# Optimization experiments

Measured on AMD Instinct MI355X. Metric: run time of the kernel, lower is better.

The kernel has to match this reference:

```python
import jax, jax.numpy as jnp
import numpy as np

ALPHA = 0.1   # leaky integration rate
NOISE = 0.02  # noise std
B, T, I, H, O = 64, 512, 128, 1024, 64


def setup_inputs() -> dict:
    key = jax.random.key(0)
    k1, k2, k3, k4, k5 = jax.random.split(key, 5)
    x = jax.random.normal(k1, (B, T, I), dtype=jnp.float32)
    wi = jax.random.normal(k2, (I, H), dtype=jnp.float32) / np.sqrt(I).astype(np.float32)
    wrec = jax.random.normal(k3, (H, H), dtype=jnp.float32) / np.sqrt(H).astype(np.float32)
    wo = jax.random.normal(k4, (H, O), dtype=jnp.float32) / np.sqrt(H).astype(np.float32)
    noise = jax.random.normal(k5, (B, T, H), dtype=jnp.float32)  # pre-sampled standard normal
    return {"x": x, "noise": noise, "wi": wi, "wrec": wrec, "wo": wo}


def reference(x, noise, wi, wrec, wo):
    # x: [B,T,I], noise: [B,T,H]; leaky tanh RNN scanned over time.
    batch = x.shape[0]
    h0 = jnp.zeros((batch, wrec.shape[0]), dtype=x.dtype)
    xs = jnp.swapaxes(x, 0, 1)       # [T,B,I]
    ns = jnpp if False else jnp.swapaxes(noise, 0, 1)  # [T,B,H]

    def step(h, inp):
        xt, nt = inp
        h = (1.0 - ALPHA) * h + ALPHA * (xt @ wi + jnp.tanh(h) @ wrec + nt * NOISE)
        return h, jnp.tanh(h) @ wo   # per-step output [B,O]

    _, outs = jax.lax.scan(step, h0, (xs, ns))  # outs: [T,B,O]
    return jnp.swapaxes(outs, 0, 1)  # [B,T,O]
```

## Files before the change

### kernel.cpp

```cpp
#include <hip/hip_runtime.h>
#include <hip/hip_bf16.h>


#define T_ 512
#define I_ 128
#define H_ 1024
#define O_ 64
#define GRPS 4
#define BG 16
#define WPG 32
#define NWG 128
#define POLL_CAP (1<<17)

#define GBUF_BYTES (GRPS*2*BG*H_*2)
#define STEPFLAG_OFF GBUF_BYTES
#define WS_NEED (GBUF_BYTES + 1024)

#define WREC_HI_E 0
#define WREC_LO_E 32768
#define WI_HI_E   65536
#define WI_LO_E   69632
#define WO_HI_E   73728
#define WO_LO_E   75776
#define RED_B     155648
#define REDO_B    161792
#define LDS_BYTES 162176

typedef __bf16 bf16x8 __attribute__((ext_vector_type(8)));
typedef float f32x4 __attribute__((ext_vector_type(4)));
typedef unsigned u32x4 __attribute__((ext_vector_type(4)));
typedef unsigned short u16;

__device__ __forceinline__ float fast_tanh(float v){
  float cx = fminf(fmaxf(v, -14.f), 14.f);
  float e = __builtin_amdgcn_exp2f(cx * 2.8853900817779268f);
  return 1.f - 2.f * __builtin_amdgcn_rcpf(e + 1.f);
}

__device__ __forceinline__ void flag_issue(unsigned& v, const u16* p){
  asm volatile("global_load_ushort %0, %1, off sc0 sc1" : "=v"(v) : "v"(p));
}
__device__ __forceinline__ unsigned sflag_load(const u16* p){
  unsigned v;
  asm volatile("global_load_ushort %0, %1, off sc0 sc1\n\ts_waitcnt vmcnt(0)"
               : "=v"(v) : "v"(p) : "memory");
  return v;
}
__device__ __forceinline__ void sflag_store(u16* p, unsigned v){
  asm volatile("global_store_short %0, %1, off sc0 sc1" :: "v"(p), "v"(v) : "memory");
}
__device__ __forceinline__ void g_load_frag(u32x4& d, const u16* p){
  asm volatile("global_load_dwordx4 %0, %1, off sc0 sc1" : "=v"(d) : "v"(p));
}
__device__ __forceinline__ void g_store_u16(u16* p, unsigned v){
  asm volatile("global_store_short %0, %1, off sc0 sc1" :: "v"(p), "v"(v) : "memory");
}
__device__ __forceinline__ void g_store_f32(float* p, float v){
  asm volatile("global_store_dword %0, %1, off" :: "v"(p), "v"(v) : "memory");
}
__device__ __forceinline__ void gl_f32x4(f32x4& d, const float* p){
  asm volatile("global_load_dwordx4 %0, %1, off" : "=v"(d) : "v"(p));
}
__device__ __forceinline__ void gl_f32(float& d, const float* p){
  asm volatile("global_load_dword %0, %1, off" : "=v"(d) : "v"(p));
}
__device__ __forceinline__ void barrier_lds(){
  asm volatile("s_waitcnt lgkmcnt(0)\n\ts_barrier" ::: "memory");
}

__device__ void load_slice(const float* __restrict__ Wg, int ld, int c0, int K,
                           __bf16* hi, __bf16* lo){
  for (int idx = threadIdx.x; idx < K*32; idx += 256){
    int k = idx >> 5, c = idx & 31;
    float v = Wg[(size_t)k*ld + c0 + c];
    __bf16 h = (__bf16)v;
    __bf16 l = (__bf16)(v - (float)h);
    int kt = k >> 5, kin = k & 31, lg = kin >> 3, j = kin & 7;
    int off = (((kt*2 + (c>>4))*64 + (lg*16 + (c&15))) << 3) + j;
    hi[off] = h; lo[off] = l;
  }
}

#define MFMA __builtin_amdgcn_mfma_f32_16x16x32_bf16
#define BC(u) __builtin_bit_cast(bf16x8, u)

#define PACKX(v0, v1, xh, xl)                                      \
  { _Pragma("unroll")                                              \
    for (int jj = 0; jj < 4; ++jj){                                \
      float aa = (v0)[jj], bb = (v1)[jj];                          \
      __bf16 ah = (__bf16)aa, bh2 = (__bf16)bb;                    \
      (xh)[jj] = ah; (xh)[jj+4] = bh2;                             \
      (xl)[jj] = (__bf16)(aa - (float)ah);                         \
      (xl)[jj+4] = (__bf16)(bb - (float)bh2); } }

extern "C" __global__ __launch_bounds__(256, 1)
void rnn_kernel(const float* __restrict__ x, const float* __restrict__ noise,
                const float* __restrict__ wi, const float* __restrict__ wrec,
                const float* __restrict__ wo, float* __restrict__ out,
                u16* __restrict__ gbuf, u16* __restrict__ sflags)
{
  extern __shared__ char smem[];
  __bf16* B = (__bf16*)smem;
  float* REDN = (float*)(smem + RED_B);
  float* REDO = (float*)(smem + REDO_B);

  const int grp  = blockIdx.x >> 5;
  const int role = blockIdx.x & 31;
  const int c0 = role * 32;

  load_slice(wrec, H_, c0, H_, B + WREC_HI_E, B + WREC_LO_E);
  load_slice(wi,   H_, c0, I_, B + WI_HI_E,  B + WI_LO_E);
  for (int idx = threadIdx.x; idx < 2*H_; idx += 256){
    int col = idx >> 10, k = idx & (H_-1);
    float v = wo[(size_t)k*O_ + role*2 + col];
    __bf16 hh = (__bf16)v;
    B[WO_HI_E + col*H_ + k] = hh;
    B[WO_LO_E + col*H_ + k] = (__bf16)(v - (float)hh);
  }
  __syncthreads();

  const int lane = threadIdx.x & 63;
  const int w    = threadIdx.x >> 6;
  const int lhalf = lane >> 4;
  const int l15   = lane & 15;
  const int bf = lane * 8;
  const int wo_off = (l15 & 1)*1024 + lhalf*8;

  u16* gg = gbuf + grp * (2*BG*H_);
  u16* gf = sflags + grp * 64;
  const u16* pollp = gf + lane;
  const u16* abase = gg + (size_t)l15*H_ + w*256 + lhalf*8;

  const float* xrow  = x + (size_t)(grp*BG + l15)*T_*I_ + lhalf*8;
  const float* nrow0 = noise + (size_t)(grp*BG + lhalf*4)*T_*H_ + c0 + (w&1)*16 + l15;
  float* orow = out + (size_t)(grp*BG + lhalf*4)*T_*O_ + role*2 + (l15 & 1);

  f32x4 h0 = {0.f,0.f,0.f,0.f};
  f32x4 xA = {0.f,0.f,0.f,0.f}, xB = {0.f,0.f,0.f,0.f};
  u32x4 a[8];
  f32x4 xv[8];
  float nz[4] = {0.f,0.f,0.f,0.f};

  if (w < 2){
    gl_f32x4(xv[0], xrow);      gl_f32x4(xv[1], xrow+4);
    gl_f32x4(xv[2], xrow+32);   gl_f32x4(xv[3], xrow+36);
    gl_f32x4(xv[4], xrow+64);   gl_f32x4(xv[5], xrow+68);
    gl_f32x4(xv[6], xrow+96);   gl_f32x4(xv[7], xrow+100);
    asm volatile("s_waitcnt vmcnt(0)"
      : "+v"(xv[0]),"+v"(xv[1]),"+v"(xv[2]),"+v"(xv[3]),
        "+v"(xv[4]),"+v"(xv[5]),"+v"(xv[6]),"+v"(xv[7]));
    __builtin_amdgcn_sched_barrier(0);
    #pragma unroll
    for (int kt = 0; kt < 4; ++kt){
      bf16x8 xh, xl; PACKX(xv[kt*2], xv[kt*2+1], xh, xl);
      bf16x8 wih = *(const bf16x8*)(B + WI_HI_E + kt*1024 + w*512 + bf);
      bf16x8 wil = *(const bf16x8*)(B + WI_LO_E + kt*1024 + w*512 + bf);
      xA = MFMA(xh, wih, xA, 0,0,0);
      xB = MFMA(xl, wih, xB, 0,0,0);
      xA = MFMA(xh, wil, xA, 0,0,0);
    }
    const float* xp = xrow + I_;
    gl_f32x4(xv[0], xp);      gl_f32x4(xv[1], xp+4);
    gl_f32x4(xv[2], xp+32);   gl_f32x4(xv[3], xp+36);
    gl_f32x4(xv[4], xp+64);   gl_f32x4(xv[5], xp+68);
    gl_f32x4(xv[6], xp+96);   gl_f32x4(xv[7], xp+100);
    gl_f32(nz[0], nrow0);
    gl_f32(nz[1], nrow0 + (size_t)T_*H_);
    gl_f32(nz[2], nrow0 + (size_t)2*T_*H_);
    gl_f32(nz[3], nrow0 + (size_t)3*T_*H_);
  }
  #pragma unroll
  for (int kt = 0; kt < 8; ++kt) g_load_frag(a[kt], abase + kt*32);

  for (int i = 0; i < T_; ++i){
    f32x4 c0A={0.f,0.f,0.f,0.f}, c0B={0.f,0.f,0.f,0.f};
    f32x4 c1A={0.f,0.f,0.f,0.f}, c1B={0.f,0.f,0.f,0.f};
    f32x4 oA ={0.f,0.f,0.f,0.f}, oB ={0.f,0.f,0.f,0.f};
    if (w == 0){ c0A = xA; c0B = xB; }
    if (w == 1){ c1A = xA; c1B = xB; }
    const int kb = w*8;
#define CSTEP(KT, N)                                                          \
    { asm volatile("s_waitcnt vmcnt(" #N ")" : "+v"(a[KT]));                  \
      __builtin_amdgcn_sched_barrier(0);                                      \
      const int kg = kb + KT;                                                 \
      bf16x8 av = BC(a[KT]);                                                  \
      bf16x8 bh0 = *(const bf16x8*)(B + WREC_HI_E + kg*1024 + bf);            \
      bf16x8 bl0 = *(const bf16x8*)(B + WREC_LO_E + kg*1024 + bf);            \
      bf16x8 bh1 = *(const bf16x8*)(B + WREC_HI_E + kg*1024 + 512 + bf);      \
      bf16x8 bl1 = *(const bf16x8*)(B + WREC_LO_E + kg*1024 + 512 + bf);      \
      bf16x8 wh  = *(const bf16x8*)(B + WO_HI_E + wo_off + kg*32);            \
      bf16x8 wl  = *(const bf16x8*)(B + WO_LO_E + wo_off + kg*32);            \
      c0A = MFMA(av, bh0, c0A, 0,0,0);  c0B = MFMA(av, bl0, c0B, 0,0,0);      \
      c1A = MFMA(av, bh1, c1A, 0,0,0);  c1B = MFMA(av, bl1, c1B, 0,0,0);      \
      oA  = MFMA(av, wh,  oA,  0,0,0);  oB  = MFMA(av, wl,  oB,  0,0,0); }
    CSTEP(0,7) CSTEP(1,6) CSTEP(2,5) CSTEP(3,4)
    CSTEP(4,3) CSTEP(5,2) CSTEP(6,1) CSTEP(7,0)
#undef CSTEP
    f32x4 cn0 = c0A + c0B, cn1 = c1A + c1B, co = oA + oB;

    if (w == 0){ *(f32x4*)&REDN[((1*3+0)*64+lane)*4] = cn1;
                 if (l15 < 2) *(f32x4*)&REDO[(0*8 + lhalf*2 + l15)*4] = co; }
    if (w == 1){ *(f32x4*)&REDN[((0*3+0)*64+lane)*4] = cn0;
                 if (l15 < 2) *(f32x4*)&REDO[(1*8 + lhalf*2 + l15)*4] = co; }
    if (w == 2){ *(f32x4*)&REDN[((0*3+1)*64+lane)*4] = cn0;
                 *(f32x4*)&REDN[((1*3+1)*64+lane)*4] = cn1; }
    if (w == 3){ *(f32x4*)&REDN[((0*3+2)*64+lane)*4] = cn0;
                 *(f32x4*)&REDN[((1*3+2)*64+lane)*4] = cn1;
                 if (l15 < 2) *(f32x4*)&REDO[(2*8 + lhalf*2 + l15)*4] = co; }
    barrier_lds();

    if (w < 2){
      const int fb = w ? 3 : 0;
      f32x4 s = w ? cn1 : cn0;
      s += *(f32x4*)&REDN[((fb+0)*64+lane)*4];
      s += *(f32x4*)&REDN[((fb+1)*64+lane)*4];
      s += *(f32x4*)&REDN[((fb+2)*64+lane)*4];
      u16* gp = gg + (size_t)((i+1)&1)*(BG*H_);
      #pragma unroll
      for (int r = 0; r < 4; ++r){
        int row = lhalf*4 + r;
        float hv = 0.9f*h0[r] + 0.1f*s[r] + 0.002f*nz[r];
        h0[r] = hv;
        u16 gv = __builtin_bit_cast(u16, (__bf16)fast_tanh(hv));
        g_store_u16(gp + (size_t)row*H_ + c0 + w*16 + l15, (unsigned)gv);
      }
    } else if (w == 2 && i > 0 && l15 < 2){
      f32x4 s = co;
      s += *(f32x4*)&REDO[(0*8 + lhalf*2 + l15)*4];
      s += *(f32x4*)&REDO[(1*8 + lhalf*2 + l15)*4];
      s += *(f32x4*)&REDO[(2*8 + lhalf*2 + l15)*4];
      #pragma unroll
      for (int r = 0; r < 4; ++r)
        g_store_f32(orow + (size_t)r*T_*O_ + (size_t)(i-1)*O_, s[r]);
    }

    if (w < 2){
      asm volatile("s_waitcnt vmcnt(0)" ::: "memory");
      if (lane == 0) sflag_store(gf + role*2 + w, (unsigned)(i+1));
    }

    unsigned pv;
    flag_issue(pv, pollp);
    if (w < 2 && i+1 < T_){
      f32x4 nxA = {0.f,0.f,0.f,0.f}, nxB = {0.f,0.f,0.f,0.f};
      #pragma unroll
      for (int kt = 0; kt < 4; ++kt){
        bf16x8 xh, xl; PACKX(xv[kt*2], xv[kt*2+1], xh, xl);
        bf16x8 wih = *(const bf16x8*)(B + WI_HI_E + kt*1024 + w*512 + bf);
        bf16x8 wil = *(const bf16x8*)(B + WI_LO_E + kt*1024 + w*512 + bf);
        nxA = MFMA(xh, wih, nxA, 0,0,0);
        nxB = MFMA(xl, wih, nxB, 0,0,0);
        nxA = MFMA(xh, wil, nxA, 0,0,0);
      }
      xA = nxA; xB = nxB;
    }
    asm volatile("s_waitcnt vmcnt(0)" : "+v"(pv));
    __builtin_amdgcn_sched_barrier(0);
    if (!__all((int)(pv >= (unsigned)(i+1)))){
      int guard = 0;
      while (true){
        unsigned v = sflag_load(pollp);
        if (__all((int)(v >= (unsigned)(i+1)))) break;
        if (++guard > POLL_CAP) break;
      }
    }
    if (w < 2){
      if (i+2 < T_){
        const float* xp = xrow + (size_t)(i+2)*I_;
        gl_f32x4(xv[0], xp);      gl_f32x4(xv[1], xp+4);
        gl_f32x4(xv[2], xp+32);   gl_f32x4(xv[3], xp+36);
        gl_f32x4(xv[4], xp+64);   gl_f32x4(xv[5], xp+68);
        gl_f32x4(xv[6], xp+96);   gl_f32x4(xv[7], xp+100);
      }
      if (i+1 < T_){
        const float* np = nrow0 + (size_t)(i+1)*H_;
        gl_f32(nz[0], np);
        gl_f32(nz[1], np + (size_t)T_*H_);
        gl_f32(nz[2], np + (size_t)2*T_*H_);
        gl_f32(nz[3], np + (size_t)3*T_*H_);
      }
    }
    {
      const u16* ap = abase + (size_t)((i+1)&1)*(BG*H_);
      #pragma unroll
      for (int kt = 0; kt < 8; ++kt) g_load_frag(a[kt], ap + kt*32);
    }
    barrier_lds();
  }

  asm volatile("s_waitcnt vmcnt(0)"
    : "+v"(a[0]),"+v"(a[1]),"+v"(a[2]),"+v"(a[3]),
      "+v"(a[4]),"+v"(a[5]),"+v"(a[6]),"+v"(a[7]));
  __builtin_amdgcn_sched_barrier(0);
  {
    f32x4 oA={0.f,0.f,0.f,0.f}, oB={0.f,0.f,0.f,0.f};
    const int kb = w*8;
    #pragma unroll
    for (int kt = 0; kt < 8; ++kt){
      const int kg = kb + kt;
      bf16x8 wh = *(const bf16x8*)(B + WO_HI_E + wo_off + kg*32);
      bf16x8 wl = *(const bf16x8*)(B + WO_LO_E + wo_off + kg*32);
      bf16x8 av = BC(a[kt]);
      oA = MFMA(av, wh, oA, 0,0,0);  oB = MFMA(av, wl, oB, 0,0,0);
    }
    f32x4 co = oA + oB;
    if (l15 < 2){
      if (w == 0) *(f32x4*)&REDO[(0*8 + lhalf*2 + l15)*4] = co;
      if (w == 1) *(f32x4*)&REDO[(1*8 + lhalf*2 + l15)*4] = co;
      if (w == 3) *(f32x4*)&REDO[(2*8 + lhalf*2 + l15)*4] = co;
    }
    barrier_lds();
    if (w == 2 && l15 < 2){
      f32x4 s = co;
      s += *(f32x4*)&REDO[(0*8 + lhalf*2 + l15)*4];
      s += *(f32x4*)&REDO[(1*8 + lhalf*2 + l15)*4];
      s += *(f32x4*)&REDO[(2*8 + lhalf*2 + l15)*4];
      #pragma unroll
      for (int r = 0; r < 4; ++r)
        g_store_f32(orow + (size_t)r*T_*O_ + (size_t)(T_-1)*O_, s[r]);
    }
  }
  asm volatile("s_waitcnt vmcnt(0)" ::: "memory");
}

extern "C" void kernel_launch(void* const* d_in, const int* in_sizes, int n_in,
                              void* d_out, int out_size, void* d_ws, size_t ws_size,
                              hipStream_t stream){
  const float* x     = (const float*)d_in[0];
  const float* noise = (const float*)d_in[1];
  const float* wi    = (const float*)d_in[2];
  const float* wrec  = (const float*)d_in[3];
  const float* wo    = (const float*)d_in[4];
  float* out = (float*)d_out;

  if (ws_size < (size_t)WS_NEED) return;
  u16* gbuf = (u16*)d_ws;
  u16* sflags = (u16*)((char*)d_ws + STEPFLAG_OFF);

  hipMemsetAsync(d_ws, 0, WS_NEED, stream);

  hipFuncSetAttribute((const void*)rnn_kernel,
                      hipFuncAttributeMaxDynamicSharedMemorySize, LDS_BYTES);

  void* args[] = {(void*)&x, (void*)&noise, (void*)&wi, (void*)&wrec, (void*)&wo,
                  (void*)&out, (void*)&gbuf, (void*)&sflags};
  hipLaunchCooperativeKernel((const void*)rnn_kernel, dim3(NWG), dim3(256),
                             args, LDS_BYTES, stream);
}
```

Before: 3.193 ms.

## Publish hidden state and step flags with 32-bit atomic swaps, move barrier

Pairs adjacent bf16 tanh outputs through a lane shuffle and writes them as 32-bit global atomic swaps, halving the number of stores. Widens the step flags to 32-bit and publishes them with an atomic swap instead of a system-coherent short store. Polling now reads one flag per lane for each wave's group of 16. The end-of-step LDS barrier is moved before the flag publish, and a barrier is added before the final output reduction. The goal is to shorten the cross-workgroup handoff latency on every timestep, at the cost of relying on atomics for coherence and adding an extra barrier to the critical path.

```diff
diff --git a/kernel.cpp b/kernel.cpp
--- a/kernel.cpp
+++ b/kernel.cpp
@@ -37,23 +37,20 @@
   return 1.f - 2.f * __builtin_amdgcn_rcpf(e + 1.f);
 }
 
-__device__ __forceinline__ void flag_issue(unsigned& v, const u16* p){
-  asm volatile("global_load_ushort %0, %1, off sc0 sc1" : "=v"(v) : "v"(p));
-}
-__device__ __forceinline__ unsigned sflag_load(const u16* p){
+__device__ __forceinline__ void flag_issue(unsigned& v, const unsigned* p){
+  asm volatile("global_load_dword %0, %1, off sc0 sc1" : "=v"(v) : "v"(p));
+}
+__device__ __forceinline__ unsigned flag_load(const unsigned* p){
   unsigned v;
-  asm volatile("global_load_ushort %0, %1, off sc0 sc1\n\ts_waitcnt vmcnt(0)"
+  asm volatile("global_load_dword %0, %1, off sc0 sc1\n\ts_waitcnt vmcnt(0)"
                : "=v"(v) : "v"(p) : "memory");
   return v;
 }
-__device__ __forceinline__ void sflag_store(u16* p, unsigned v){
-  asm volatile("global_store_short %0, %1, off sc0 sc1" :: "v"(p), "v"(v) : "memory");
+__device__ __forceinline__ void atom_swap_u32(unsigned* p, unsigned v){
+  asm volatile("global_atomic_swap %0, %1, off" :: "v"(p), "v"(v) : "memory");
 }
 __device__ __forceinline__ void g_load_frag(u32x4& d, const u16* p){
   asm volatile("global_load_dwordx4 %0, %1, off sc0 sc1" : "=v"(d) : "v"(p));
-}
-__device__ __forceinline__ void g_store_u16(u16* p, unsigned v){
-  asm volatile("global_store_short %0, %1, off sc0 sc1" :: "v"(p), "v"(v) : "memory");
 }
 __device__ __forceinline__ void g_store_f32(float* p, float v){
   asm volatile("global_store_dword %0, %1, off" :: "v"(p), "v"(v) : "memory");
@@ -97,7 +94,7 @@
 void rnn_kernel(const float* __restrict__ x, const float* __restrict__ noise,
                 const float* __restrict__ wi, const float* __restrict__ wrec,
                 const float* __restrict__ wo, float* __restrict__ out,
-                u16* __restrict__ gbuf, u16* __restrict__ sflags)
+                u16* __restrict__ gbuf, unsigned* __restrict__ flags)
 {
   extern __shared__ char smem[];
   __bf16* B = (__bf16*)smem;
@@ -127,8 +124,9 @@
   const int wo_off = (l15 & 1)*1024 + lhalf*8;
 
   u16* gg = gbuf + grp * (2*BG*H_);
-  u16* gf = sflags + grp * 64;
-  const u16* pollp = gf + lane;
+  unsigned* gfl = flags + grp * 64;
+  const unsigned* pollp = gfl + w*16 + (lane & 15);
+  unsigned* myflag = gfl + role*2 + w;
   const u16* abase = gg + (size_t)l15*H_ + w*256 + lhalf*8;
 
   const float* xrow  = x + (size_t)(grp*BG + l15)*T_*I_ + lhalf*8;
@@ -216,13 +214,21 @@
       s += *(f32x4*)&REDN[((fb+1)*64+lane)*4];
       s += *(f32x4*)&REDN[((fb+2)*64+lane)*4];
       u16* gp = gg + (size_t)((i+1)&1)*(BG*H_);
+      unsigned pk[4];
       #pragma unroll
       for (int r = 0; r < 4; ++r){
-        int row = lhalf*4 + r;
         float hv = 0.9f*h0[r] + 0.1f*s[r] + 0.002f*nz[r];
         h0[r] = hv;
-        u16 gv = __builtin_bit_cast(u16, (__bf16)fast_tanh(hv));
-        g_store_u16(gp + (size_t)row*H_ + c0 + w*16 + l15, (unsigned)gv);
+        unsigned gv = (unsigned)__builtin_bit_cast(u16, (__bf16)fast_tanh(hv));
+        unsigned pg = (unsigned)__shfl_xor((int)gv, 1);
+        pk[r] = gv | (pg << 16);
+      }
+      if (!(l15 & 1)){
+        #pragma unroll
+        for (int r = 0; r < 4; ++r){
+          int row = lhalf*4 + r;
+          atom_swap_u32((unsigned*)(gp + (size_t)row*H_ + c0 + w*16 + l15), pk[r]);
+        }
       }
     } else if (w == 2 && i > 0 && l15 < 2){
       f32x4 s = co;
@@ -233,10 +239,11 @@
       for (int r = 0; r < 4; ++r)
         g_store_f32(orow + (size_t)r*T_*O_ + (size_t)(i-1)*O_, s[r]);
     }
+    barrier_lds();
 
     if (w < 2){
       asm volatile("s_waitcnt vmcnt(0)" ::: "memory");
-      if (lane == 0) sflag_store(gf + role*2 + w, (unsigned)(i+1));
+      if (lane == 0) atom_swap_u32(myflag, (unsigned)(i+1));
     }
 
     unsigned pv;
@@ -259,7 +266,7 @@
     if (!__all((int)(pv >= (unsigned)(i+1)))){
       int guard = 0;
       while (true){
-        unsigned v = sflag_load(pollp);
+        unsigned v = flag_load(pollp);
         if (__all((int)(v >= (unsigned)(i+1)))) break;
         if (++guard > POLL_CAP) break;
       }
@@ -285,7 +292,6 @@
       #pragma unroll
       for (int kt = 0; kt < 8; ++kt) g_load_frag(a[kt], ap + kt*32);
     }
-    barrier_lds();
   }
 
   asm volatile("s_waitcnt vmcnt(0)"
@@ -304,6 +310,7 @@
       oA = MFMA(av, wh, oA, 0,0,0);  oB = MFMA(av, wl, oB, 0,0,0);
     }
     f32x4 co = oA + oB;
+    barrier_lds();
     if (l15 < 2){
       if (w == 0) *(f32x4*)&REDO[(0*8 + lhalf*2 + l15)*4] = co;
       if (w == 1) *(f32x4*)&REDO[(1*8 + lhalf*2 + l15)*4] = co;
@@ -335,7 +342,7 @@
 
   if (ws_size < (size_t)WS_NEED) return;
   u16* gbuf = (u16*)d_ws;
-  u16* sflags = (u16*)((char*)d_ws + STEPFLAG_OFF);
+  unsigned* flags = (unsigned*)((char*)d_ws + STEPFLAG_OFF);
 
   hipMemsetAsync(d_ws, 0, WS_NEED, stream);
 
@@ -343,7 +350,7 @@
                       hipFuncAttributeMaxDynamicSharedMemorySize, LDS_BYTES);
 
   void* args[] = {(void*)&x, (void*)&noise, (void*)&wi, (void*)&wrec, (void*)&wo,
-                  (void*)&out, (void*)&gbuf, (void*)&sflags};
+                  (void*)&out, (void*)&gbuf, (void*)&flags};
   hipLaunchCooperativeKernel((const void*)rnn_kernel, dim3(NWG), dim3(256),
                              args, LDS_BYTES, stream);
 }
```

After: 3.182 ms. Within noise of the previous version (-0.3%).

## Restructure per-step schedule: wait for all h fragments, move x/noise prefetch earlier

Applied to the files above, without the earlier changes.

Replaces the staggered per-fragment vmcnt waits with a single wait for all eight recurrent-state fragments at the top of each step. The x and noise loads for the next step are issued right after the MFMA loop, and the input projection runs after the flag store. Each wave role (state producers, output writer, others) gets its own poll-and-reload path, and the output store is deferred until after the next h fragments are issued. The goal is a shorter critical path between steps, at the cost of losing the overlap between arriving fragments and the MFMAs.

```diff
diff --git a/kernel.cpp b/kernel.cpp
--- a/kernel.cpp
+++ b/kernel.cpp
@@ -8,7 +8,6 @@
 #define O_ 64
 #define GRPS 4
 #define BG 16
-#define WPG 32
 #define NWG 128
 #define POLL_CAP (1<<17)
 
@@ -50,7 +49,7 @@
   asm volatile("global_store_short %0, %1, off sc0 sc1" :: "v"(p), "v"(v) : "memory");
 }
 __device__ __forceinline__ void g_load_frag(u32x4& d, const u16* p){
-  asm volatile("global_load_dwordx4 %0, %1, off sc0 sc1" : "=v"(d) : "v"(p));
+  asm volatile("global_load_dwordx4 %0, %1, off sc0 sc1" : "=v"(d) : "v"(p) : "memory");
 }
 __device__ __forceinline__ void g_store_u16(u16* p, unsigned v){
   asm volatile("global_store_short %0, %1, off sc0 sc1" :: "v"(p), "v"(v) : "memory");
@@ -93,6 +92,21 @@
       (xl)[jj] = (__bf16)(aa - (float)ah);                         \
       (xl)[jj+4] = (__bf16)(bb - (float)bh2); } }
 
+#define SEEDS(OA, OB)                                                          \
+  { f32x4 nxA = {0.f,0.f,0.f,0.f}, nxB = {0.f,0.f,0.f,0.f};                    \
+    _Pragma("unroll")                                                          \
+    for (int kt = 0; kt < 4; ++kt){                                            \
+      f32x4 v0 = (kt==0)?xv0:(kt==1)?xv2:(kt==2)?xv4:xv6;                      \
+      f32x4 v1 = (kt==0)?xv1:(kt==1)?xv3:(kt==2)?xv5:xv7;                      \
+      bf16x8 xh, xl; PACKX(v0, v1, xh, xl);                                    \
+      bf16x8 wih = *(const bf16x8*)(B + WI_HI_E + kt*1024 + w*512 + bf);       \
+      bf16x8 wil = *(const bf16x8*)(B + WI_LO_E + kt*1024 + w*512 + bf);       \
+      nxA = MFMA(xh, wih, nxA, 0,0,0);                                         \
+      nxB = MFMA(xl, wih, nxB, 0,0,0);                                         \
+      nxA = MFMA(xh, wil, nxA, 0,0,0);                                         \
+    }                                                                          \
+    OA = nxA; OB = nxB; }
+
 extern "C" __global__ __launch_bounds__(256, 1)
 void rnn_kernel(const float* __restrict__ x, const float* __restrict__ noise,
                 const float* __restrict__ wi, const float* __restrict__ wrec,
@@ -138,65 +152,71 @@
   f32x4 h0 = {0.f,0.f,0.f,0.f};
   f32x4 xA = {0.f,0.f,0.f,0.f}, xB = {0.f,0.f,0.f,0.f};
   u32x4 a[8];
-  f32x4 xv[8];
+  f32x4 xv0,xv1,xv2,xv3,xv4,xv5,xv6,xv7;
   float nz[4] = {0.f,0.f,0.f,0.f};
 
   if (w < 2){
-    gl_f32x4(xv[0], xrow);      gl_f32x4(xv[1], xrow+4);
-    gl_f32x4(xv[2], xrow+32);   gl_f32x4(xv[3], xrow+36);
-    gl_f32x4(xv[4], xrow+64);   gl_f32x4(xv[5], xrow+68);
-    gl_f32x4(xv[6], xrow+96);   gl_f32x4(xv[7], xrow+100);
-    asm volatile("s_waitcnt vmcnt(0)"
-      : "+v"(xv[0]),"+v"(xv[1]),"+v"(xv[2]),"+v"(xv[3]),
-        "+v"(xv[4]),"+v"(xv[5]),"+v"(xv[6]),"+v"(xv[7]));
-    __builtin_amdgcn_sched_barrier(0);
-    #pragma unroll
-    for (int kt = 0; kt < 4; ++kt){
-      bf16x8 xh, xl; PACKX(xv[kt*2], xv[kt*2+1], xh, xl);
-      bf16x8 wih = *(const bf16x8*)(B + WI_HI_E + kt*1024 + w*512 + bf);
-      bf16x8 wil = *(const bf16x8*)(B + WI_LO_E + kt*1024 + w*512 + bf);
-      xA = MFMA(xh, wih, xA, 0,0,0);
-      xB = MFMA(xl, wih, xB, 0,0,0);
-      xA = MFMA(xh, wil, xA, 0,0,0);
-    }
-    const float* xp = xrow + I_;
-    gl_f32x4(xv[0], xp);      gl_f32x4(xv[1], xp+4);
-    gl_f32x4(xv[2], xp+32);   gl_f32x4(xv[3], xp+36);
-    gl_f32x4(xv[4], xp+64);   gl_f32x4(xv[5], xp+68);
-    gl_f32x4(xv[6], xp+96);   gl_f32x4(xv[7], xp+100);
+    gl_f32x4(xv0, xrow);      gl_f32x4(xv1, xrow+4);
+    gl_f32x4(xv2, xrow+32);   gl_f32x4(xv3, xrow+36);
+    gl_f32x4(xv4, xrow+64);   gl_f32x4(xv5, xrow+68);
+    gl_f32x4(xv6, xrow+96);   gl_f32x4(xv7, xrow+100);
     gl_f32(nz[0], nrow0);
     gl_f32(nz[1], nrow0 + (size_t)T_*H_);
-    gl_f32(nz[2], nrow0 + (size_t)2*T_*H_);
-    gl_f32(nz[3], nrow0 + (size_t)3*T_*H_);
+    gl_f32(nz[2], nrow0 + 2*(size_t)T_*H_);
+    gl_f32(nz[3], nrow0 + 3*(size_t)T_*H_);
+    asm volatile("s_waitcnt vmcnt(0)"
+      : "+v"(xv0),"+v"(xv1),"+v"(xv2),"+v"(xv3),
+        "+v"(xv4),"+v"(xv5),"+v"(xv6),"+v"(xv7),
+        "+v"(nz[0]),"+v"(nz[1]),"+v"(nz[2]),"+v"(nz[3]) :: "memory");
+    __builtin_amdgcn_sched_barrier(0);
+    SEEDS(xA, xB);
   }
   #pragma unroll
   for (int kt = 0; kt < 8; ++kt) g_load_frag(a[kt], abase + kt*32);
+  barrier_lds();
 
   for (int i = 0; i < T_; ++i){
+    asm volatile("s_waitcnt vmcnt(0)"
+      : "+v"(a[0]),"+v"(a[1]),"+v"(a[2]),"+v"(a[3]),
+        "+v"(a[4]),"+v"(a[5]),"+v"(a[6]),"+v"(a[7]) :: "memory");
+    __builtin_amdgcn_sched_barrier(0);
+
     f32x4 c0A={0.f,0.f,0.f,0.f}, c0B={0.f,0.f,0.f,0.f};
     f32x4 c1A={0.f,0.f,0.f,0.f}, c1B={0.f,0.f,0.f,0.f};
     f32x4 oA ={0.f,0.f,0.f,0.f}, oB ={0.f,0.f,0.f,0.f};
     if (w == 0){ c0A = xA; c0B = xB; }
     if (w == 1){ c1A = xA; c1B = xB; }
     const int kb = w*8;
-#define CSTEP(KT, N)                                                          \
-    { asm volatile("s_waitcnt vmcnt(" #N ")" : "+v"(a[KT]));                  \
-      __builtin_amdgcn_sched_barrier(0);                                      \
-      const int kg = kb + KT;                                                 \
-      bf16x8 av = BC(a[KT]);                                                  \
-      bf16x8 bh0 = *(const bf16x8*)(B + WREC_HI_E + kg*1024 + bf);            \
-      bf16x8 bl0 = *(const bf16x8*)(B + WREC_LO_E + kg*1024 + bf);            \
-      bf16x8 bh1 = *(const bf16x8*)(B + WREC_HI_E + kg*1024 + 512 + bf);      \
-      bf16x8 bl1 = *(const bf16x8*)(B + WREC_LO_E + kg*1024 + 512 + bf);      \
-      bf16x8 wh  = *(const bf16x8*)(B + WO_HI_E + wo_off + kg*32);            \
-      bf16x8 wl  = *(const bf16x8*)(B + WO_LO_E + wo_off + kg*32);            \
-      c0A = MFMA(av, bh0, c0A, 0,0,0);  c0B = MFMA(av, bl0, c0B, 0,0,0);      \
-      c1A = MFMA(av, bh1, c1A, 0,0,0);  c1B = MFMA(av, bl1, c1B, 0,0,0);      \
-      oA  = MFMA(av, wh,  oA,  0,0,0);  oB  = MFMA(av, wl,  oB,  0,0,0); }
-    CSTEP(0,7) CSTEP(1,6) CSTEP(2,5) CSTEP(3,4)
-    CSTEP(4,3) CSTEP(5,2) CSTEP(6,1) CSTEP(7,0)
-#undef CSTEP
+    #pragma unroll
+    for (int kt = 0; kt < 8; ++kt){
+      const int kg = kb + kt;
+      bf16x8 bh0 = *(const bf16x8*)(B + WREC_HI_E + kg*1024 + bf);
+      bf16x8 bl0 = *(const bf16x8*)(B + WREC_LO_E + kg*1024 + bf);
+      bf16x8 bh1 = *(const bf16x8*)(B + WREC_HI_E + kg*1024 + 512 + bf);
+      bf16x8 bl1 = *(const bf16x8*)(B + WREC_LO_E + kg*1024 + 512 + bf);
+      bf16x8 wh  = *(const bf16x8*)(B + WO_HI_E + wo_off + kg*32);
+      bf16x8 wl  = *(const bf16x8*)(B + WO_LO_E + wo_off + kg*32);
+      bf16x8 av = BC(a[kt]);
+      c0A = MFMA(av, bh0, c0A, 0,0,0);  c0B = MFMA(av, bl0, c0B, 0,0,0);
+      c1A = MFMA(av, bh1, c1A, 0,0,0);  c1B = MFMA(av, bl1, c1B, 0,0,0);
+      oA  = MFMA(av, wh,  oA,  0,0,0);  oB  = MFMA(av, wl,  oB,  0,0,0);
+    }
     f32x4 cn0 = c0A + c0B, cn1 = c1A + c1B, co = oA + oB;
+
+    float nz2[4] = {0.f,0.f,0.f,0.f};
+    const bool more = (i+1 < T_);
+    if (w < 2 && more){
+      const float* xp = xrow + (size_t)(i+1)*I_;
+      gl_f32x4(xv0, xp);      gl_f32x4(xv1, xp+4);
+      gl_f32x4(xv2, xp+32);   gl_f32x4(xv3, xp+36);
+      gl_f32x4(xv4, xp+64);   gl_f32x4(xv5, xp+68);
+      gl_f32x4(xv6, xp+96);   gl_f32x4(xv7, xp+100);
+      const float* np = nrow0 + (size_t)(i+1)*H_;
+      gl_f32(nz2[0], np);
+      gl_f32(nz2[1], np + (size_t)T_*H_);
+      gl_f32(nz2[2], np + 2*(size_t)T_*H_);
+      gl_f32(nz2[3], np + 3*(size_t)T_*H_);
+    }
 
     if (w == 0){ *(f32x4*)&REDN[((1*3+0)*64+lane)*4] = cn1;
                  if (l15 < 2) *(f32x4*)&REDO[(0*8 + lhalf*2 + l15)*4] = co; }
@@ -209,6 +229,7 @@
                  if (l15 < 2) *(f32x4*)&REDO[(2*8 + lhalf*2 + l15)*4] = co; }
     barrier_lds();
 
+    const unsigned tgt = (unsigned)(i+1);
     if (w < 2){
       const int fb = w ? 3 : 0;
       f32x4 s = w ? cn1 : cn0;
@@ -224,73 +245,90 @@
         u16 gv = __builtin_bit_cast(u16, (__bf16)fast_tanh(hv));
         g_store_u16(gp + (size_t)row*H_ + c0 + w*16 + l15, (unsigned)gv);
       }
-    } else if (w == 2 && i > 0 && l15 < 2){
-      f32x4 s = co;
-      s += *(f32x4*)&REDO[(0*8 + lhalf*2 + l15)*4];
-      s += *(f32x4*)&REDO[(1*8 + lhalf*2 + l15)*4];
-      s += *(f32x4*)&REDO[(2*8 + lhalf*2 + l15)*4];
-      #pragma unroll
-      for (int r = 0; r < 4; ++r)
-        g_store_f32(orow + (size_t)r*T_*O_ + (size_t)(i-1)*O_, s[r]);
-    }
-
-    if (w < 2){
-      asm volatile("s_waitcnt vmcnt(0)" ::: "memory");
-      if (lane == 0) sflag_store(gf + role*2 + w, (unsigned)(i+1));
-    }
-
-    unsigned pv;
-    flag_issue(pv, pollp);
-    if (w < 2 && i+1 < T_){
-      f32x4 nxA = {0.f,0.f,0.f,0.f}, nxB = {0.f,0.f,0.f,0.f};
-      #pragma unroll
-      for (int kt = 0; kt < 4; ++kt){
-        bf16x8 xh, xl; PACKX(xv[kt*2], xv[kt*2+1], xh, xl);
-        bf16x8 wih = *(const bf16x8*)(B + WI_HI_E + kt*1024 + w*512 + bf);
-        bf16x8 wil = *(const bf16x8*)(B + WI_LO_E + kt*1024 + w*512 + bf);
-        nxA = MFMA(xh, wih, nxA, 0,0,0);
-        nxB = MFMA(xl, wih, nxB, 0,0,0);
-        nxA = MFMA(xh, wil, nxA, 0,0,0);
-      }
-      xA = nxA; xB = nxB;
-    }
-    asm volatile("s_waitcnt vmcnt(0)" : "+v"(pv));
-    __builtin_amdgcn_sched_barrier(0);
-    if (!__all((int)(pv >= (unsigned)(i+1)))){
-      int guard = 0;
-      while (true){
-        unsigned v = sflag_load(pollp);
-        if (__all((int)(v >= (unsigned)(i+1)))) break;
-        if (++guard > POLL_CAP) break;
-      }
-    }
-    if (w < 2){
-      if (i+2 < T_){
-        const float* xp = xrow + (size_t)(i+2)*I_;
-        gl_f32x4(xv[0], xp);      gl_f32x4(xv[1], xp+4);
-        gl_f32x4(xv[2], xp+32);   gl_f32x4(xv[3], xp+36);
-        gl_f32x4(xv[4], xp+64);   gl_f32x4(xv[5], xp+68);
-        gl_f32x4(xv[6], xp+96);   gl_f32x4(xv[7], xp+100);
-      }
-      if (i+1 < T_){
-        const float* np = nrow0 + (size_t)(i+1)*H_;
-        gl_f32(nz[0], np);
-        gl_f32(nz[1], np + (size_t)T_*H_);
-        gl_f32(nz[2], np + (size_t)2*T_*H_);
-        gl_f32(nz[3], np + (size_t)3*T_*H_);
-      }
-    }
-    {
-      const u16* ap = abase + (size_t)((i+1)&1)*(BG*H_);
-      #pragma unroll
-      for (int kt = 0; kt < 8; ++kt) g_load_frag(a[kt], ap + kt*32);
-    }
+      if (more){
+        asm volatile("s_waitcnt vmcnt(0)"
+          : "+v"(xv0),"+v"(xv1),"+v"(xv2),"+v"(xv3),
+            "+v"(xv4),"+v"(xv5),"+v"(xv6),"+v"(xv7),
+            "+v"(nz2[0]),"+v"(nz2[1]),"+v"(nz2[2]),"+v"(nz2[3]) :: "memory");
+      } else {
+        asm volatile("s_waitcnt vmcnt(0)" ::: "memory");
+      }
+      __builtin_amdgcn_sched_barrier(0);
+      if (lane == 0) sflag_store(gf + role*2 + w, tgt);
+      unsigned pv; flag_issue(pv, pollp);
+      if (more){ SEEDS(xA, xB); }
+      nz[0]=nz2[0]; nz[1]=nz2[1]; nz[2]=nz2[2]; nz[3]=nz2[3];
+      asm volatile("s_waitcnt vmcnt(0)" : "+v"(pv) :: "memory");
+      __builtin_amdgcn_sched_barrier(0);
+      if (!__all((int)(pv >= tgt))){
+        int guard = 0;
+        while (true){
+          unsigned v = sflag_load(pollp);
+          if (__all((int)(v >= tgt))) break;
+          if (++guard > POLL_CAP) break;
+        }
+      }
+      {
+        const u16* ap = abase + (size_t)((i+1)&1)*(BG*H_);
+        #pragma unroll
+        for (int kt = 0; kt < 8; ++kt) g_load_frag(a[kt], ap + kt*32);
+      }
+    } else if (w == 2){
+      f32x4 so = {0.f,0.f,0.f,0.f};
+      bool do_out = false;
+      if (i > 0){
+        f32x4 s = co;
+        s += *(f32x4*)&REDO[(0*8 + lhalf*2 + l15)*4];
+        s += *(f32x4*)&REDO[(1*8 + lhalf*2 + l15)*4];
+        s += *(f32x4*)&REDO[(2*8 + lhalf*2 + l15)*4];
+        so = s; do_out = (l15 < 2);
+      }
+      unsigned pv; flag_issue(pv, pollp);
+      asm volatile("s_waitcnt vmcnt(0)" : "+v"(pv) :: "memory");
+      __builtin_amdgcn_sched_barrier(0);
+      if (!__all((int)(pv >= tgt))){
+        int guard = 0;
+        while (true){
+          unsigned v = sflag_load(pollp);
+          if (__all((int)(v >= tgt))) break;
+          if (++guard > POLL_CAP) break;
+        }
+      }
+      {
+        const u16* ap = abase + (size_t)((i+1)&1)*(BG*H_);
+        #pragma unroll
+        for (int kt = 0; kt < 8; ++kt) g_load_frag(a[kt], ap + kt*32);
+      }
+      if (do_out){
+        #pragma unroll
+        for (int r = 0; r < 4; ++r)
+          g_store_f32(orow + (size_t)r*T_*O_ + (size_t)(i-1)*O_, so[r]);
+      }
+    } else {
+      unsigned pv; flag_issue(pv, pollp);
+      asm volatile("s_waitcnt vmcnt(0)" : "+v"(pv) :: "memory");
+      __builtin_amdgcn_sched_barrier(0);
+      if (!__all((int)(pv >= tgt))){
+        int guard = 0;
+        while (true){
+          unsigned v = sflag_load(pollp);
+          if (__all((int)(v >= tgt))) break;
+          if (++guard > POLL_CAP) break;
+        }
+      }
+      {
+        const u16* ap = abase + (size_t)((i+1)&1)*(BG*H_);
+        #pragma unroll
+        for (int kt = 0; kt < 8; ++kt) g_load_frag(a[kt], ap + kt*32);
+      }
+    }
+
     barrier_lds();
   }
 
   asm volatile("s_waitcnt vmcnt(0)"
     : "+v"(a[0]),"+v"(a[1]),"+v"(a[2]),"+v"(a[3]),
-      "+v"(a[4]),"+v"(a[5]),"+v"(a[6]),"+v"(a[7]));
+      "+v"(a[4]),"+v"(a[5]),"+v"(a[6]),"+v"(a[7]) :: "memory");
   __builtin_amdgcn_sched_barrier(0);
   {
     f32x4 oA={0.f,0.f,0.f,0.f}, oB={0.f,0.f,0.f,0.f};
```

Result: faster. 2.776 ms (-13.1%).
